# Kernel tuning notes

Hardware: AMD Instinct MI355X
Metric: run time of the kernel (lower is better)

The kernel has to match this reference:

```python
import jax, jax.numpy as jnp
import numpy as np

S = 14
C = 20
STEP = 1.0 / 14
LAMBDA_COORD = 3.0
LAMBDA_NOOBJ = 0.3
LAMBDA_OBJ = 1.0
LAMBDA_CLS = 1.5


def setup_inputs() -> dict:
    key = jax.random.key(0)
    k1, k2 = jax.random.split(key)
    batch = 4096
    pred = jax.random.normal(k1, (batch, S, S, 30), dtype=jnp.float32)
    target = jax.random.normal(k2, (batch, S, S, 30), dtype=jnp.float32)
    return {"pred": pred, "target": target}


def _convert_boxes(box):
    # box: [B, S, S, 2, 4] in (cx, cy, w, h) grid-relative coords
    # grid index i is the x (third) axis, j the y (second) axis, per forward's [x, y]
    gi = jnp.arange(S, dtype=box.dtype)[None, None, :, None]  # x index
    gj = jnp.arange(S, dtype=box.dtype)[None, :, None, None]  # y index
    x = (box[..., 0] + gi) * STEP - box[..., 2] * 0.5
    y = (box[..., 1] + gj) * STEP - box[..., 3] * 0.5
    out = jnp.stack([x, y, box[..., 2], box[..., 3]], axis=-1)
    return jnp.maximum(out, 0.0)  # torch.clamp(box, min=0) on the whole box


def _iou(b1, b2):
    x1, y1, w1, h1 = b1[..., 0], b1[..., 1], b1[..., 2], b1[..., 3]
    x2, y2, w2, h2 = b2[..., 0], b2[..., 1], b2[..., 2], b2[..., 3]
    inter_w = jnp.maximum(w1 + w2 - (jnp.maximum(x1 + w1, x2 + w2) - jnp.minimum(x1, x2)), 0.0)
    inter_h = jnp.maximum(h1 + h2 - (jnp.maximum(y1 + h1, y2 + h2) - jnp.minimum(y1, y2)), 0.0)
    inter = inter_w * inter_h
    union = w1 * h1 + w2 * h2 - inter
    return inter / (union + 1e-6)


def _smooth_l1_sum(p, t, mask):
    d = p - t
    ad = jnp.abs(d)
    l = jnp.where(ad < 1.0, 0.5 * d * d, ad - 0.5)
    return jnp.sum(l * mask)


def reference(pred, target):
    batch = pred.shape[0]
    pb = pred[..., :10].reshape(batch, S, S, 2, 5)
    tb = target[..., :10].reshape(batch, S, S, 2, 5)
    pred_cls = pred[..., 10:]
    target_cls = target[..., 10:]

    obj_mask = tb[..., 4] > 0          # [B,S,S,2]
    sig_mask = obj_mask[..., 1]         # [B,S,S]

    # responsible-box selection: elementwise IoU between pred box k and target box k
    ious = _iou(_convert_boxes(pb[..., :4]), _convert_boxes(tb[..., :4]))  # [B,S,S,2]
    max_i = jnp.argmax(ious, axis=-1)   # first-max, matches torch .max(0)
    keep = jnp.arange(2) == max_i[..., None]
    obj_mask = jnp.where(sig_mask[..., None], obj_mask & keep, obj_mask)
    noobj_mask = ~obj_mask

    om = obj_mask.astype(pred.dtype)
    nm = noobj_mask.astype(pred.dtype)

    conf_sq = (pb[..., 4] - tb[..., 4]) ** 2
    noobj_loss = jnp.sum(conf_sq * nm)
    obj_loss = jnp.sum(conf_sq * om)

    xy_loss = _smooth_l1_sum(pb[..., :2], tb[..., :2], om[..., None])
    wh_loss = _smooth_l1_sum(
        jnp.sqrt(jnp.maximum(pb[..., 2:4], 1e-6)),
        jnp.sqrt(jnp.maximum(tb[..., 2:4], 1e-6)),
        om[..., None],
    )

    logp = jax.nn.log_softmax(pred_cls, axis=-1)
    tgt_idx = jnp.argmax(target_cls, axis=-1)  # [B,S,S]
    nll = -jnp.take_along_axis(logp, tgt_idx[..., None], axis=-1)[..., 0]
    class_loss = jnp.sum(nll * sig_mask.astype(pred.dtype))

    total = (LAMBDA_COORD * (xy_loss + wh_loss)
             + LAMBDA_OBJ * obj_loss
             + LAMBDA_NOOBJ * noobj_loss
             + LAMBDA_CLS * class_loss) / batch
    return total
```

## Files before the change

kernel.cpp:

```cpp
#include <hip/hip_runtime.h>
#include <math.h>

#define SS 14
#define NCLS 20
#define CELL_FLOATS 30

__device__ __forceinline__ float smooth_l1(float d) {
    float ad = fabsf(d);
    return ad < 1.0f ? 0.5f * d * d : ad - 0.5f;
}

__device__ __forceinline__ void conv_box(const float* b, float gi, float gj,
                                         float& x, float& y, float& w, float& h) {
    const float STEP = 1.0f / 14.0f;
    x = fmaxf((b[0] + gi) * STEP - b[2] * 0.5f, 0.0f);
    y = fmaxf((b[1] + gj) * STEP - b[3] * 0.5f, 0.0f);
    w = fmaxf(b[2], 0.0f);
    h = fmaxf(b[3], 0.0f);
}

__device__ __forceinline__ float iou_box(float x1, float y1, float w1, float h1,
                                         float x2, float y2, float w2, float h2) {
    float iw = fmaxf(w1 + w2 - (fmaxf(x1 + w1, x2 + w2) - fminf(x1, x2)), 0.0f);
    float ih = fmaxf(h1 + h2 - (fmaxf(y1 + h1, y2 + h2) - fminf(y1, y2)), 0.0f);
    float inter = iw * ih;
    float uni = w1 * h1 + w2 * h2 - inter;
    return inter / (uni + 1e-6f);
}

__global__ void zero_out_kernel(float* out) { out[0] = 0.0f; }

__global__ __launch_bounds__(256) void yolo_loss_kernel(
    const float* __restrict__ pred, const float* __restrict__ target,
    float* __restrict__ out, int ncells, float inv_batch) {
    int cell = blockIdx.x * blockDim.x + threadIdx.x;
    float tot = 0.0f;
    if (cell < ncells) {
        float p[CELL_FLOATS], t[CELL_FLOATS];
        const float2* pp = (const float2*)(pred + (size_t)cell * CELL_FLOATS);
        const float2* tp = (const float2*)(target + (size_t)cell * CELL_FLOATS);
#pragma unroll
        for (int k = 0; k < CELL_FLOATS / 2; ++k) {
            ((float2*)p)[k] = pp[k];
            ((float2*)t)[k] = tp[k];
        }

        int rc = cell % (SS * SS);
        float gj = (float)(rc / SS);
        float gi = (float)(rc % SS);

        float px, py, pw, ph, tx, ty, tw, th;
        conv_box(p + 0, gi, gj, px, py, pw, ph);
        conv_box(t + 0, gi, gj, tx, ty, tw, th);
        float iou0 = iou_box(px, py, pw, ph, tx, ty, tw, th);
        conv_box(p + 5, gi, gj, px, py, pw, ph);
        conv_box(t + 5, gi, gj, tx, ty, tw, th);
        float iou1 = iou_box(px, py, pw, ph, tx, ty, tw, th);

        bool obj0 = t[4] > 0.0f;
        bool obj1 = t[9] > 0.0f;
        bool sig = obj1;
        bool m1 = iou1 > iou0;
        bool om0 = sig ? (obj0 && !m1) : obj0;
        bool om1 = sig ? m1 : false;

        float c0 = p[4] - t[4]; c0 *= c0;
        float c1 = p[9] - t[9]; c1 *= c1;
        float obj_l = (om0 ? c0 : 0.0f) + (om1 ? c1 : 0.0f);
        float noobj_l = (om0 ? 0.0f : c0) + (om1 ? 0.0f : c1);

        float xy = 0.0f, wh = 0.0f;
        if (om0) {
            xy += smooth_l1(p[0] - t[0]) + smooth_l1(p[1] - t[1]);
            wh += smooth_l1(sqrtf(fmaxf(p[2], 1e-6f)) - sqrtf(fmaxf(t[2], 1e-6f)));
            wh += smooth_l1(sqrtf(fmaxf(p[3], 1e-6f)) - sqrtf(fmaxf(t[3], 1e-6f)));
        }
        if (om1) {
            xy += smooth_l1(p[5] - t[5]) + smooth_l1(p[6] - t[6]);
            wh += smooth_l1(sqrtf(fmaxf(p[7], 1e-6f)) - sqrtf(fmaxf(t[7], 1e-6f)));
            wh += smooth_l1(sqrtf(fmaxf(p[8], 1e-6f)) - sqrtf(fmaxf(t[8], 1e-6f)));
        }

        float cls = 0.0f;
        {
            float m = p[10];
#pragma unroll
            for (int c = 1; c < NCLS; ++c) m = fmaxf(m, p[10 + c]);
            float se = 0.0f;
#pragma unroll
            for (int c = 0; c < NCLS; ++c) se += expf(p[10 + c] - m);
            float bt = t[10];
            int bi = 0;
#pragma unroll
            for (int c = 1; c < NCLS; ++c) {
                if (t[10 + c] > bt) { bt = t[10 + c]; bi = c; }
            }
            float logp = p[10 + bi] - m - logf(se);
            cls = sig ? -logp : 0.0f;
        }

        tot = 3.0f * (xy + wh) + obj_l + 0.3f * noobj_l + 1.5f * cls;
        tot *= inv_batch;
    }

#pragma unroll
    for (int off = 32; off > 0; off >>= 1) tot += __shfl_down(tot, off, 64);
    __shared__ float wsum[4];
    int lane = threadIdx.x & 63;
    int wid = threadIdx.x >> 6;
    if (lane == 0) wsum[wid] = tot;
    __syncthreads();
    if (threadIdx.x == 0) {
        float s = wsum[0] + wsum[1] + wsum[2] + wsum[3];
        atomicAdd(out, s);
    }
}

extern "C" void kernel_launch(void* const* d_in, const int* in_sizes, int n_in,
                              void* d_out, int out_size, void* d_ws, size_t ws_size,
                              hipStream_t stream) {
    const float* pred = (const float*)d_in[0];
    const float* target = (const float*)d_in[1];
    float* out = (float*)d_out;

    int total = in_sizes[0];
    int ncells = total / CELL_FLOATS;
    int batch = ncells / (SS * SS);
    float inv_batch = 1.0f / (float)batch;

    zero_out_kernel<<<1, 1, 0, stream>>>(out);
    int block = 256;
    int grid = (ncells + block - 1) / block;
    yolo_loss_kernel<<<grid, block, 0, stream>>>(pred, target, out, ncells, inv_batch);
}
```

Measured before the change: 235.0 us.

## Stage per-block cell data through LDS with coalesced float4 loads

Each block now cooperatively loads its 256 cells of pred and target into shared memory using contiguous float4 reads, synchronizes, then each thread reads its own cell from LDS. This replaces strided per-thread float2 global loads at a 120-byte stride, which coalesced poorly. In exchange it uses about 61 KB of LDS per block, which limits occupancy, and adds bank conflicts on the strided LDS reads.

```diff
diff --git a/kernel.cpp b/kernel.cpp
--- a/kernel.cpp
+++ b/kernel.cpp
@@ -4,6 +4,10 @@
 #define SS 14
 #define NCLS 20
 #define CELL_FLOATS 30
+#define BLOCK 256
+#define CELLS_PER_BLOCK 256
+#define FPB (CELLS_PER_BLOCK * CELL_FLOATS)
+#define F4PB (FPB / 4)
 
 __device__ __forceinline__ float smooth_l1(float d) {
     float ad = fabsf(d);
@@ -30,15 +34,33 @@
 
 __global__ void zero_out_kernel(float* out) { out[0] = 0.0f; }
 
-__global__ __launch_bounds__(256) void yolo_loss_kernel(
-    const float* __restrict__ pred, const float* __restrict__ target,
+__global__ __launch_bounds__(BLOCK) void yolo_loss_kernel(
+    const float4* __restrict__ pred4, const float4* __restrict__ target4,
     float* __restrict__ out, int ncells, float inv_batch) {
-    int cell = blockIdx.x * blockDim.x + threadIdx.x;
+    __shared__ float sp[FPB];
+    __shared__ float st[FPB];
+
+    const int tid = threadIdx.x;
+    const int cell0 = blockIdx.x * CELLS_PER_BLOCK;
+    const long long total4 = ((long long)ncells * CELL_FLOATS) / 4;
+    const long long base4 = (long long)blockIdx.x * F4PB;
+
+#pragma unroll
+    for (int k = 0; k < 8; ++k) {
+        int i = tid + k * BLOCK;
+        if (i < F4PB && base4 + i < total4) {
+            ((float4*)sp)[i] = pred4[base4 + i];
+            ((float4*)st)[i] = target4[base4 + i];
+        }
+    }
+    __syncthreads();
+
+    int cell = cell0 + tid;
     float tot = 0.0f;
     if (cell < ncells) {
         float p[CELL_FLOATS], t[CELL_FLOATS];
-        const float2* pp = (const float2*)(pred + (size_t)cell * CELL_FLOATS);
-        const float2* tp = (const float2*)(target + (size_t)cell * CELL_FLOATS);
+        const float2* pp = (const float2*)(sp + tid * CELL_FLOATS);
+        const float2* tp = (const float2*)(st + tid * CELL_FLOATS);
 #pragma unroll
         for (int k = 0; k < CELL_FLOATS / 2; ++k) {
             ((float2*)p)[k] = pp[k];
@@ -119,8 +141,8 @@
 extern "C" void kernel_launch(void* const* d_in, const int* in_sizes, int n_in,
                               void* d_out, int out_size, void* d_ws, size_t ws_size,
                               hipStream_t stream) {
-    const float* pred = (const float*)d_in[0];
-    const float* target = (const float*)d_in[1];
+    const float4* pred4 = (const float4*)d_in[0];
+    const float4* target4 = (const float4*)d_in[1];
     float* out = (float*)d_out;
 
     int total = in_sizes[0];
@@ -129,7 +151,6 @@
     float inv_batch = 1.0f / (float)batch;
 
     zero_out_kernel<<<1, 1, 0, stream>>>(out);
-    int block = 256;
-    int grid = (ncells + block - 1) / block;
-    yolo_loss_kernel<<<grid, block, 0, stream>>>(pred, target, out, ncells, inv_batch);
+    int grid = (ncells + CELLS_PER_BLOCK - 1) / CELLS_PER_BLOCK;
+    yolo_loss_kernel<<<grid, BLOCK, 0, stream>>>(pred4, target4, out, ncells, inv_batch);
 }
```

Measured after the change: 234.2 us. About the same (-0.3%).

## Stage cells through LDS with coalesced float4 loads, prefetch, and two-pass reduction

Applied to the files above, without the earlier changes.

The kernel now runs a fixed grid of single-wavefront blocks. Each block walks over 64-cell chunks, loading each chunk with coalesced float4/float2 reads into LDS and prefetching the next chunk into registers while it computes the current one. Per-block partial sums go to a workspace, and a single-block reduce kernel adds them and also handles tail cells, which removes the atomic and the zeroing kernel. It also swaps expf/logf for the fast __expf/__logf intrinsics, which lowers accuracy slightly. The block-to-LDS writes are not followed by a barrier, which relies on a 64-thread block being a single wavefront.

```diff
diff --git a/kernel.cpp b/kernel.cpp
--- a/kernel.cpp
+++ b/kernel.cpp
@@ -4,6 +4,10 @@
 #define SS 14
 #define NCLS 20
 #define CELL_FLOATS 30
+#define CHUNK 64
+#define FPC (CHUNK * CELL_FLOATS)
+#define F4PC (FPC / 4)
+#define NBLOCKS 1792
 
 __device__ __forceinline__ float smooth_l1(float d) {
     float ad = fabsf(d);
@@ -28,92 +32,158 @@
     return inter / (uni + 1e-6f);
 }
 
-__global__ void zero_out_kernel(float* out) { out[0] = 0.0f; }
-
-__global__ __launch_bounds__(256) void yolo_loss_kernel(
+__device__ __forceinline__ float cell_loss(const float* __restrict__ p,
+                                           const float* __restrict__ t, int cell) {
+    int rc = cell % (SS * SS);
+    float gj = (float)(rc / SS);
+    float gi = (float)(rc % SS);
+
+    float px, py, pw, ph, tx, ty, tw, th;
+    conv_box(p + 0, gi, gj, px, py, pw, ph);
+    conv_box(t + 0, gi, gj, tx, ty, tw, th);
+    float iou0 = iou_box(px, py, pw, ph, tx, ty, tw, th);
+    conv_box(p + 5, gi, gj, px, py, pw, ph);
+    conv_box(t + 5, gi, gj, tx, ty, tw, th);
+    float iou1 = iou_box(px, py, pw, ph, tx, ty, tw, th);
+
+    bool obj0 = t[4] > 0.0f;
+    bool obj1 = t[9] > 0.0f;
+    bool sig = obj1;
+    bool m1 = iou1 > iou0;
+    bool om0 = sig ? (obj0 && !m1) : obj0;
+    bool om1 = sig ? m1 : false;
+
+    float c0 = p[4] - t[4]; c0 *= c0;
+    float c1 = p[9] - t[9]; c1 *= c1;
+    float obj_l = (om0 ? c0 : 0.0f) + (om1 ? c1 : 0.0f);
+    float noobj_l = (om0 ? 0.0f : c0) + (om1 ? 0.0f : c1);
+
+    float xy = 0.0f, wh = 0.0f;
+    if (om0) {
+        xy += smooth_l1(p[0] - t[0]) + smooth_l1(p[1] - t[1]);
+        wh += smooth_l1(sqrtf(fmaxf(p[2], 1e-6f)) - sqrtf(fmaxf(t[2], 1e-6f)));
+        wh += smooth_l1(sqrtf(fmaxf(p[3], 1e-6f)) - sqrtf(fmaxf(t[3], 1e-6f)));
+    }
+    if (om1) {
+        xy += smooth_l1(p[5] - t[5]) + smooth_l1(p[6] - t[6]);
+        wh += smooth_l1(sqrtf(fmaxf(p[7], 1e-6f)) - sqrtf(fmaxf(t[7], 1e-6f)));
+        wh += smooth_l1(sqrtf(fmaxf(p[8], 1e-6f)) - sqrtf(fmaxf(t[8], 1e-6f)));
+    }
+
+    float cls = 0.0f;
+    {
+        float m = p[10];
+#pragma unroll
+        for (int c = 1; c < NCLS; ++c) m = fmaxf(m, p[10 + c]);
+        float se = 0.0f;
+#pragma unroll
+        for (int c = 0; c < NCLS; ++c) se += __expf(p[10 + c] - m);
+        float bt = t[10];
+        int bi = 0;
+#pragma unroll
+        for (int c = 1; c < NCLS; ++c) {
+            if (t[10 + c] > bt) { bt = t[10 + c]; bi = c; }
+        }
+        float logp = p[10 + bi] - m - __logf(se);
+        cls = sig ? -logp : 0.0f;
+    }
+
+    return 3.0f * (xy + wh) + obj_l + 0.3f * noobj_l + 1.5f * cls;
+}
+
+#define CHUNK_LOADS(chunk)                                                    \
+    {                                                                         \
+        long long b4 = (long long)(chunk) * F4PC + l;                         \
+        p0 = pred4[b4];        q0 = target4[b4];                              \
+        p1 = pred4[b4 + 64];   q1 = target4[b4 + 64];                         \
+        p2 = pred4[b4 + 128];  q2 = target4[b4 + 128];                        \
+        p3 = pred4[b4 + 192];  q3 = target4[b4 + 192];                        \
+        p4 = pred4[b4 + 256];  q4 = target4[b4 + 256];                        \
+        p5 = pred4[b4 + 320];  q5 = target4[b4 + 320];                        \
+        p6 = pred4[b4 + 384];  q6 = target4[b4 + 384];                        \
+        long long b2 = (long long)(chunk) * (FPC / 2) + 896 + l;              \
+        p7 = pred2[b2];        q7 = target2[b2];                              \
+    }
+
+__global__ __launch_bounds__(64) void yolo_loss_kernel(
+    const float4* __restrict__ pred4, const float4* __restrict__ target4,
+    const float2* __restrict__ pred2, const float2* __restrict__ target2,
+    float* __restrict__ partials, int nchunks, int cpw, float inv_batch) {
+    __shared__ __align__(16) float sp[FPC];
+    __shared__ __align__(16) float st[FPC];
+    float4* sp4 = (float4*)sp; float2* sp2 = (float2*)sp;
+    float4* st4 = (float4*)st; float2* st2 = (float2*)st;
+
+    const int l = threadIdx.x;
+    const int c0 = blockIdx.x * cpw;
+    float acc = 0.0f;
+
+    float4 p0, p1, p2, p3, p4, p5, p6; float2 p7;
+    float4 q0, q1, q2, q3, q4, q5, q6; float2 q7;
+
+    if (c0 < nchunks) {
+        CHUNK_LOADS(c0);
+
+        for (int j = 0; j < cpw; ++j) {
+            int chunk = c0 + j;
+            if (chunk >= nchunks) break;
+
+            sp4[l] = p0;        st4[l] = q0;
+            sp4[l + 64] = p1;   st4[l + 64] = q1;
+            sp4[l + 128] = p2;  st4[l + 128] = q2;
+            sp4[l + 192] = p3;  st4[l + 192] = q3;
+            sp4[l + 256] = p4;  st4[l + 256] = q4;
+            sp4[l + 320] = p5;  st4[l + 320] = q5;
+            sp4[l + 384] = p6;  st4[l + 384] = q6;
+            sp2[896 + l] = p7;  st2[896 + l] = q7;
+
+            if (j + 1 < cpw && chunk + 1 < nchunks) CHUNK_LOADS(chunk + 1);
+
+            float p[CELL_FLOATS], t[CELL_FLOATS];
+            const float2* pr = sp2 + l * (CELL_FLOATS / 2);
+            const float2* tr = st2 + l * (CELL_FLOATS / 2);
+#pragma unroll
+            for (int m = 0; m < CELL_FLOATS / 2; ++m) {
+                ((float2*)p)[m] = pr[m];
+                ((float2*)t)[m] = tr[m];
+            }
+
+            acc += cell_loss(p, t, chunk * CHUNK + l);
+        }
+    }
+
+    acc *= inv_batch;
+#pragma unroll
+    for (int off = 32; off > 0; off >>= 1) acc += __shfl_down(acc, off, 64);
+    if (l == 0) partials[blockIdx.x] = acc;
+}
+
+__global__ __launch_bounds__(256) void reduce_kernel(
+    const float* __restrict__ partials, int n,
     const float* __restrict__ pred, const float* __restrict__ target,
-    float* __restrict__ out, int ncells, float inv_batch) {
-    int cell = blockIdx.x * blockDim.x + threadIdx.x;
-    float tot = 0.0f;
-    if (cell < ncells) {
+    int tail_start, int tail_cnt, float inv_batch, float* __restrict__ out) {
+    float s = 0.0f;
+    for (int i = threadIdx.x; i < n; i += 256) s += partials[i];
+    for (int i = threadIdx.x; i < tail_cnt; i += 256) {
+        int cell = tail_start + i;
         float p[CELL_FLOATS], t[CELL_FLOATS];
         const float2* pp = (const float2*)(pred + (size_t)cell * CELL_FLOATS);
         const float2* tp = (const float2*)(target + (size_t)cell * CELL_FLOATS);
 #pragma unroll
-        for (int k = 0; k < CELL_FLOATS / 2; ++k) {
-            ((float2*)p)[k] = pp[k];
-            ((float2*)t)[k] = tp[k];
+        for (int m = 0; m < CELL_FLOATS / 2; ++m) {
+            ((float2*)p)[m] = pp[m];
+            ((float2*)t)[m] = tp[m];
         }
-
-        int rc = cell % (SS * SS);
-        float gj = (float)(rc / SS);
-        float gi = (float)(rc % SS);
-
-        float px, py, pw, ph, tx, ty, tw, th;
-        conv_box(p + 0, gi, gj, px, py, pw, ph);
-        conv_box(t + 0, gi, gj, tx, ty, tw, th);
-        float iou0 = iou_box(px, py, pw, ph, tx, ty, tw, th);
-        conv_box(p + 5, gi, gj, px, py, pw, ph);
-        conv_box(t + 5, gi, gj, tx, ty, tw, th);
-        float iou1 = iou_box(px, py, pw, ph, tx, ty, tw, th);
-
-        bool obj0 = t[4] > 0.0f;
-        bool obj1 = t[9] > 0.0f;
-        bool sig = obj1;
-        bool m1 = iou1 > iou0;
-        bool om0 = sig ? (obj0 && !m1) : obj0;
-        bool om1 = sig ? m1 : false;
-
-        float c0 = p[4] - t[4]; c0 *= c0;
-        float c1 = p[9] - t[9]; c1 *= c1;
-        float obj_l = (om0 ? c0 : 0.0f) + (om1 ? c1 : 0.0f);
-        float noobj_l = (om0 ? 0.0f : c0) + (om1 ? 0.0f : c1);
-
-        float xy = 0.0f, wh = 0.0f;
-        if (om0) {
-            xy += smooth_l1(p[0] - t[0]) + smooth_l1(p[1] - t[1]);
-            wh += smooth_l1(sqrtf(fmaxf(p[2], 1e-6f)) - sqrtf(fmaxf(t[2], 1e-6f)));
-            wh += smooth_l1(sqrtf(fmaxf(p[3], 1e-6f)) - sqrtf(fmaxf(t[3], 1e-6f)));
-        }
-        if (om1) {
-            xy += smooth_l1(p[5] - t[5]) + smooth_l1(p[6] - t[6]);
-            wh += smooth_l1(sqrtf(fmaxf(p[7], 1e-6f)) - sqrtf(fmaxf(t[7], 1e-6f)));
-            wh += smooth_l1(sqrtf(fmaxf(p[8], 1e-6f)) - sqrtf(fmaxf(t[8], 1e-6f)));
-        }
-
-        float cls = 0.0f;
-        {
-            float m = p[10];
-#pragma unroll
-            for (int c = 1; c < NCLS; ++c) m = fmaxf(m, p[10 + c]);
-            float se = 0.0f;
-#pragma unroll
-            for (int c = 0; c < NCLS; ++c) se += expf(p[10 + c] - m);
-            float bt = t[10];
-            int bi = 0;
-#pragma unroll
-            for (int c = 1; c < NCLS; ++c) {
-                if (t[10 + c] > bt) { bt = t[10 + c]; bi = c; }
-            }
-            float logp = p[10 + bi] - m - logf(se);
-            cls = sig ? -logp : 0.0f;
-        }
-
-        tot = 3.0f * (xy + wh) + obj_l + 0.3f * noobj_l + 1.5f * cls;
-        tot *= inv_batch;
-    }
-
-#pragma unroll
-    for (int off = 32; off > 0; off >>= 1) tot += __shfl_down(tot, off, 64);
+        s += cell_loss(p, t, cell) * inv_batch;
+    }
+#pragma unroll
+    for (int off = 32; off > 0; off >>= 1) s += __shfl_down(s, off, 64);
     __shared__ float wsum[4];
     int lane = threadIdx.x & 63;
     int wid = threadIdx.x >> 6;
-    if (lane == 0) wsum[wid] = tot;
+    if (lane == 0) wsum[wid] = s;
     __syncthreads();
-    if (threadIdx.x == 0) {
-        float s = wsum[0] + wsum[1] + wsum[2] + wsum[3];
-        atomicAdd(out, s);
-    }
+    if (threadIdx.x == 0) out[0] = wsum[0] + wsum[1] + wsum[2] + wsum[3];
 }
 
 extern "C" void kernel_launch(void* const* d_in, const int* in_sizes, int n_in,
@@ -122,14 +192,22 @@
     const float* pred = (const float*)d_in[0];
     const float* target = (const float*)d_in[1];
     float* out = (float*)d_out;
+    float* partials = (float*)d_ws;
 
     int total = in_sizes[0];
     int ncells = total / CELL_FLOATS;
     int batch = ncells / (SS * SS);
     float inv_batch = 1.0f / (float)batch;
 
-    zero_out_kernel<<<1, 1, 0, stream>>>(out);
-    int block = 256;
-    int grid = (ncells + block - 1) / block;
-    yolo_loss_kernel<<<grid, block, 0, stream>>>(pred, target, out, ncells, inv_batch);
-}
+    int nchunks = ncells / CHUNK;
+    int tail_start = nchunks * CHUNK;
+    int tail_cnt = ncells - tail_start;
+    int cpw = (nchunks + NBLOCKS - 1) / NBLOCKS;
+
+    yolo_loss_kernel<<<NBLOCKS, 64, 0, stream>>>(
+        (const float4*)pred, (const float4*)target,
+        (const float2*)pred, (const float2*)target,
+        partials, nchunks, cpw, inv_batch);
+    reduce_kernel<<<1, 256, 0, stream>>>(partials, NBLOCKS, pred, target,
+                                         tail_start, tail_cnt, inv_batch, out);
+}
```

Measured after the change: 222.5 us. -5.3%, faster.
